# Kernel tuning notes

Measured on AMD Instinct MI355X. Metric: run time of the kernel, lower is better.

Reference implementation:

```python
import jax, jax.numpy as jnp
import numpy as np

DIM = 1024
HEADS = 16
HDIM = DIM // HEADS
MLP_HID = 4096
LN_EPS = 1e-5
NORM_EPS = 1e-12  # F.normalize eps


def _layernorm(x, g, b):
    mu = jnp.mean(x, axis=-1, keepdims=True)
    var = jnp.mean(jnp.square(x - mu), axis=-1, keepdims=True)
    return (x - mu) / jnp.sqrt(var + LN_EPS) * g + b


def _l2norm(x):
    n = jnp.linalg.norm(x, axis=-1, keepdims=True)
    return x / jnp.maximum(n, NORM_EPS)


def setup_inputs() -> dict:
    key = jax.random.key(0)
    ks = jax.random.split(key, 8)
    s = 0.02
    x = jax.random.normal(ks[0], (2, 2048, DIM), dtype=jnp.float32)
    w_qkv = jax.random.normal(ks[1], (3 * DIM, DIM), dtype=jnp.float32) * s  # torch Linear weight (out,in)
    w_proj = jax.random.normal(ks[2], (DIM, DIM), dtype=jnp.float32) * s
    temp = jnp.ones((HEADS, 1, 1), dtype=jnp.float32)
    w1 = jax.random.normal(ks[3], (MLP_HID, DIM), dtype=jnp.float32) * s
    b1 = jnp.zeros((MLP_HID,), dtype=jnp.float32)
    w2 = jax.random.normal(ks[4], (DIM, MLP_HID), dtype=jnp.float32) * s
    b2 = jnp.zeros((DIM,), dtype=jnp.float32)
    ln1_g = jnp.ones((DIM,), dtype=jnp.float32)
    ln1_b = jnp.zeros((DIM,), dtype=jnp.float32)
    ln2_g = jnp.ones((DIM,), dtype=jnp.float32)
    ln2_b = jnp.zeros((DIM,), dtype=jnp.float32)
    return {"x": x, "ln1_g": ln1_g, "ln1_b": ln1_b, "w_qkv": w_qkv,
            "w_proj": w_proj, "temp": temp, "ln2_g": ln2_g, "ln2_b": ln2_b,
            "w1": w1, "b1": b1, "w2": w2, "b2": b2}


def reference(x, ln1_g, ln1_b, w_qkv, w_proj, temp, ln2_g, ln2_b, w1, b1, w2, b2):
    b, n, c = x.shape
    # --- MHSA with L2-normalized q,k and learnable per-head temperature ---
    h = _layernorm(x, ln1_g, ln1_b)
    qkv = h @ w_qkv.T                             # [b,n,3c]
    qkv = qkv.reshape(b, n, 3, HEADS, HDIM).transpose(2, 0, 3, 1, 4)  # [3,b,h,n,d]
    q, k, v = qkv[0], qkv[1], qkv[2]
    q = _l2norm(q)
    k = _l2norm(k)
    attn = jnp.einsum('bhnd,bhmd->bhnm', q, k) * temp  # temp [h,1,1] broadcasts
    attn = jax.nn.softmax(attn, axis=-1)
    out = jnp.einsum('bhnm,bhmd->bhnd', attn, v)       # [b,h,n,d]
    out = out.transpose(0, 2, 1, 3).reshape(b, n, c)
    x = x + out @ w_proj.T
    # --- MLP ---
    h = _layernorm(x, ln2_g, ln2_b)
    h = jax.nn.gelu(h @ w1.T + b1, approximate=False)
    x = x + h @ w2.T + b2
    return x
```

## Files before the change

### kernel.cpp

```cpp
#include <hip/hip_runtime.h>
#include <cstdint>
#include <cstddef>

typedef unsigned short u16;
typedef __attribute__((ext_vector_type(8))) short short8;
typedef __attribute__((ext_vector_type(4))) float f32x4;
typedef __attribute__((ext_vector_type(4))) float float4v;
typedef __attribute__((ext_vector_type(4))) u16 u16x4;

__device__ __forceinline__ u16 f2bf(float f) {
  union { float f; uint32_t u; } v; v.f = f;
  uint32_t u = v.u;
  return (u16)((u + 0x7FFFu + ((u >> 16) & 1u)) >> 16);
}
__device__ __forceinline__ float bf2f(u16 s) {
  union { uint32_t u; float f; } v; v.u = ((uint32_t)s) << 16; return v.f;
}

__device__ __forceinline__ float fast_exp2(float x) {
#if __has_builtin(__builtin_amdgcn_exp2f)
  return __builtin_amdgcn_exp2f(x);
#else
  return exp2f(x);
#endif
}

__device__ __forceinline__ void gload16(const u16* g, u16* l) {
  __builtin_amdgcn_global_load_lds((const __attribute__((address_space(1))) void*)g,
                                   (__attribute__((address_space(3))) void*)l,
                                   16, 0, 0);
}

__global__ __launch_bounds__(256) void k_cvt(const float* __restrict__ in, u16* __restrict__ out, int n4) {
  int i = blockIdx.x * 256 + threadIdx.x;
  if (i >= n4) return;
  float4v v = *(const float4v*)(in + (size_t)i * 4);
  u16x4 o;
  #pragma unroll
  for (int j = 0; j < 4; j++) o[j] = f2bf(v[j]);
  *(u16x4*)(out + (size_t)i * 4) = o;
}

__global__ __launch_bounds__(256) void k_ln(const float* __restrict__ x, const float* __restrict__ g,
                                            const float* __restrict__ b, u16* __restrict__ out) {
  int row = blockIdx.x, tid = threadIdx.x;
  int wid = tid >> 6;
  const float* xr = x + (size_t)row * 1024;
  float4v v = *(const float4v*)(xr + tid * 4);
  float s = v[0] + v[1] + v[2] + v[3];
  float sq = v[0]*v[0] + v[1]*v[1] + v[2]*v[2] + v[3]*v[3];
  #pragma unroll
  for (int m = 1; m <= 32; m <<= 1) { s += __shfl_xor(s, m); sq += __shfl_xor(sq, m); }
  __shared__ float ss[4], ssq[4];
  if ((tid & 63) == 0) { ss[wid] = s; ssq[wid] = sq; }
  __syncthreads();
  s = ss[0] + ss[1] + ss[2] + ss[3];
  sq = ssq[0] + ssq[1] + ssq[2] + ssq[3];
  float mu = s * (1.0f/1024.0f);
  float var = sq * (1.0f/1024.0f) - mu*mu;
  float rs = rsqrtf(var + 1e-5f);
  u16x4 o;
  #pragma unroll
  for (int j = 0; j < 4; j++) {
    float y = (v[j] - mu) * rs * g[tid*4+j] + b[tid*4+j];
    o[j] = f2bf(y);
  }
  *(u16x4*)(out + (size_t)row * 1024 + tid * 4) = o;
}

__global__ __launch_bounds__(256) void k_redln(const float* __restrict__ x, const u16* __restrict__ P,
                                               const float* __restrict__ g, const float* __restrict__ b,
                                               float* __restrict__ x1, u16* __restrict__ h2) {
  int row = blockIdx.x, tid = threadIdx.x;
  int wid = tid >> 6;
  size_t off = (size_t)row * 1024 + tid * 4;
  float4v v = *(const float4v*)(x + off);
  #pragma unroll
  for (int z = 0; z < 4; z++) {
    u16x4 p = *(const u16x4*)(P + (size_t)z * 4194304 + off);
    #pragma unroll
    for (int j = 0; j < 4; j++) v[j] += bf2f(p[j]);
  }
  *(float4v*)(x1 + off) = v;
  float s = v[0] + v[1] + v[2] + v[3];
  float sq = v[0]*v[0] + v[1]*v[1] + v[2]*v[2] + v[3]*v[3];
  #pragma unroll
  for (int m = 1; m <= 32; m <<= 1) { s += __shfl_xor(s, m); sq += __shfl_xor(sq, m); }
  __shared__ float ss[4], ssq[4];
  if ((tid & 63) == 0) { ss[wid] = s; ssq[wid] = sq; }
  __syncthreads();
  s = ss[0] + ss[1] + ss[2] + ss[3];
  sq = ssq[0] + ssq[1] + ssq[2] + ssq[3];
  float mu = s * (1.0f/1024.0f);
  float var = sq * (1.0f/1024.0f) - mu*mu;
  float rs = rsqrtf(var + 1e-5f);
  u16x4 o;
  #pragma unroll
  for (int j = 0; j < 4; j++) o[j] = f2bf((v[j] - mu) * rs * g[tid*4+j] + b[tid*4+j]);
  *(u16x4*)(h2 + off) = o;
}

template<int EPI>
__global__ __launch_bounds__(512, 2) void k_g256(const u16* __restrict__ A, const u16* __restrict__ B,
                                                 const float* __restrict__ bias, u16* __restrict__ Cb,
                                                 int M, int N, int K, int Ksub) {
  extern __shared__ __align__(16) u16 smem[];
  int tid = threadIdx.x;
  int gx = gridDim.x;
  int lin = blockIdx.y * gx + blockIdx.x;
  int nwg = gx * gridDim.y;
  int cpx = nwg >> 3;
  int swz = (lin & 7) * cpx + (lin >> 3);
  int bx = swz % gx, by = swz / gx;
  int m0 = by * 256, n0 = bx * 256;
  int kbase = blockIdx.z * Ksub;
  int wid = tid >> 6, lane = tid & 63;
  int wm = wid >> 2, wn = wid & 3;
  int l15 = lane & 15, l16 = lane >> 4;

  f32x4 acc[8][4] = {};
  int nt = Ksub >> 5;

  auto STAGE = [&](int bsel, int kb) {
    u16* abase = smem + bsel * 16384;
    u16* bbase = abase + 8192;
    #pragma unroll
    for (int i = 0; i < 2; i++) {
      int c = i*512 + tid;
      int R = c >> 3, p = c & 7;
      int sp = p ^ (R & 7);
      int r = 2*R + (sp >> 2);
      int g = sp & 3;
      gload16(A + (size_t)(m0 + r)*K + kb + g*8, abase + c*8);
      gload16(B + (size_t)(n0 + r)*K + kb + g*8, bbase + c*8);
    }
  };

  STAGE(0, kbase);

  for (int t = 0; t < nt; ++t) {
    int sl = t & 1;
    asm volatile("s_waitcnt vmcnt(0)" ::: "memory");
    __builtin_amdgcn_sched_barrier(0);
    __builtin_amdgcn_s_barrier();
    __builtin_amdgcn_sched_barrier(0);
    if (t + 1 < nt) STAGE(sl ^ 1, kbase + (t + 1) * 32);
    const u16* ab = smem + sl * 16384;
    const u16* bb = ab + 8192;
    short8 af[8], bf[4];
    #pragma unroll
    for (int mf = 0; mf < 8; mf++) {
      int r = wm*128 + mf*16 + l15;
      int R = r >> 1;
      int sp = ((r & 1)*4 + l16) ^ (R & 7);
      af[mf] = *(const short8*)(ab + R*64 + sp*8);
    }
    #pragma unroll
    for (int nf = 0; nf < 4; nf++) {
      int r = wn*64 + nf*16 + l15;
      int R = r >> 1;
      int sp = ((r & 1)*4 + l16) ^ (R & 7);
      bf[nf] = *(const short8*)(bb + R*64 + sp*8);
    }
    asm volatile("s_waitcnt lgkmcnt(0)" ::: "memory");
    __builtin_amdgcn_sched_barrier(0);
    __builtin_amdgcn_s_setprio(1);
    #pragma unroll
    for (int mf = 0; mf < 8; mf++)
      #pragma unroll
      for (int nf = 0; nf < 4; nf++)
        acc[mf][nf] = __builtin_amdgcn_mfma_f32_16x16x32_bf16(af[mf], bf[nf], acc[mf][nf], 0, 0, 0);
    __builtin_amdgcn_s_setprio(0);
  }

  size_t zoff = (EPI == 6) ? (size_t)blockIdx.z * M * N : 0;
  #pragma unroll
  for (int mf = 0; mf < 8; mf++) {
    #pragma unroll
    for (int nf = 0; nf < 4; nf++) {
      int col = n0 + wn*64 + nf*16 + l15;
      #pragma unroll
      for (int r = 0; r < 4; r++) {
        int row = m0 + wm*128 + mf*16 + l16*4 + r;
        float v = acc[mf][nf][r];
        if constexpr (EPI == 2) { v += bias[col]; v = 0.5f*v*(1.0f + erff(v*0.70710678118f)); }
        Cb[zoff + (size_t)row*N + col] = f2bf(v);
      }
    }
  }
}

template<int HASB>
__global__ __launch_bounds__(256) void k_red4(const float* __restrict__ base, const float* __restrict__ bias,
                                              const u16* __restrict__ P, float* __restrict__ out) {
  int i = blockIdx.x * 256 + threadIdx.x;
  float4v v = *(const float4v*)(base + (size_t)i * 4);
  if constexpr (HASB) {
    float4v bb = *(const float4v*)(bias + (size_t)(i & 255) * 4);
    #pragma unroll
    for (int j = 0; j < 4; j++) v[j] += bb[j];
  }
  #pragma unroll
  for (int z = 0; z < 4; z++) {
    u16x4 p = *(const u16x4*)(P + (size_t)z * 4194304 + (size_t)i * 4);
    #pragma unroll
    for (int j = 0; j < 4; j++) v[j] += bf2f(p[j]);
  }
  *(float4v*)(out + (size_t)i * 4) = v;
}

__global__ __launch_bounds__(256) void k_prep(const u16* __restrict__ qkv, const float* __restrict__ temp,
                                              u16* __restrict__ Qn, u16* __restrict__ Kn, u16* __restrict__ Vt) {
  int grp = blockIdx.x, bh = blockIdx.y;
  int b = bh >> 4, h = bh & 15;
  int tid = threadIdx.x, wid = tid >> 6, lane = tid & 63;
  int n0 = grp * 64;
  __shared__ __align__(16) u16 vs[64*64];
  float tmp = temp[h] * 1.44269504f;
  for (int j = 0; j < 16; j++) {
    int tl = wid + 4*j;
    size_t roff = (size_t)((b*2048) + n0 + tl) * 3072;
    float q = bf2f(qkv[roff + h*64 + lane]);
    float k = bf2f(qkv[roff + 1024 + h*64 + lane]);
    u16 vraw = qkv[roff + 2048 + h*64 + lane];
    float sq = q*q, sk = k*k;
    #pragma unroll
    for (int m = 1; m <= 32; m <<= 1) { sq += __shfl_xor(sq, m); sk += __shfl_xor(sk, m); }
    float qs = tmp / fmaxf(sqrtf(sq), 1e-12f);
    float ksc = 1.0f / fmaxf(sqrtf(sk), 1e-12f);
    size_t obase = ((size_t)bh*2048 + n0 + tl)*64 + lane;
    Qn[obase] = f2bf(q * qs);
    Kn[obase] = f2bf(k * ksc);
    vs[tl*64 + lane] = vraw;
  }
  __syncthreads();
  int d = tid & 63, chunk = tid >> 6;
  u16 vals[16];
  #pragma unroll
  for (int jj = 0; jj < 16; jj++) vals[jj] = vs[(chunk*16 + jj)*64 + d];
  short8 w0, w1v;
  #pragma unroll
  for (int j = 0; j < 8; j++) { w0[j] = (short)vals[j]; w1v[j] = (short)vals[8+j]; }
  size_t vo = ((size_t)bh*64 + d)*2048 + n0 + chunk*16;
  *(short8*)(Vt + vo) = w0;
  *(short8*)(Vt + vo + 8) = w1v;
}

__device__ __forceinline__ int akey(int row) { return (row & 3) | (((row >> 3) & 1) << 2); }

__global__ __launch_bounds__(256) void k_attn(const u16* __restrict__ Qn, const u16* __restrict__ Kn,
                                              const u16* __restrict__ Vt, const float* __restrict__ temp,
                                              u16* __restrict__ Out) {
  __shared__ __align__(16) u16 Ks[2][64*64];
  __shared__ __align__(16) u16 Vs[2][64*64];
  int lin = blockIdx.y * gridDim.x + blockIdx.x;
  int c = lin & 7, t5 = lin >> 3;
  int bh = c*4 + (t5 >> 4);
  int qg = t5 & 15;
  int b = bh >> 4, h = bh & 15;
  int tid = threadIdx.x, wid = tid >> 6, lane = tid & 63;
  int l15 = lane & 15, l16 = lane >> 4;
  size_t base = (size_t)bh * 2048 * 64;
  size_t vbase = (size_t)bh * 64 * 2048;
  int q0 = qg*128 + wid*32;
  float m2 = fabsf(temp[h]) * 1.44269504f;
  short8 qf[2][2];
  #pragma unroll
  for (int g = 0; g < 2; g++)
    #pragma unroll
    for (int ks = 0; ks < 2; ks++)
      qf[g][ks] = *(const short8*)(Qn + base + (size_t)(q0 + g*16 + l15)*64 + ks*32 + l16*8);
  f32x4 o[2][4] = {};
  float lrow[2] = {0.f, 0.f};
  int prow = (l15 & 3) + 8*(l15 >> 2);

  auto STAGE = [&](int bsel, int kv0) {
    #pragma unroll
    for (int i = 0; i < 2; i++) {
      int cc = i*256 + tid;
      int row = cc >> 3, p = cc & 7;
      int g = p ^ akey(row);
      gload16(Kn + base + (size_t)(kv0 + row)*64 + g*8, &Ks[bsel][(i*256 + wid*64)*8]);
      gload16(Vt + vbase + (size_t)row*2048 + kv0 + g*8, &Vs[bsel][(i*256 + wid*64)*8]);
    }
  };

  STAGE(0, 0);
  __syncthreads();
  int cur = 0;
  for (int kv0 = 0; kv0 < 2048; kv0 += 64) {
    if (kv0 + 64 < 2048) STAGE(cur ^ 1, kv0 + 64);
    f32x4 s[2][4] = {};
    #pragma unroll
    for (int dks = 0; dks < 2; dks++) {
      #pragma unroll
      for (int ss = 0; ss < 4; ss++) {
        int row = (ss & 1)*4 + (ss >> 1)*32 + prow;
        short8 kf = *(const short8*)&Ks[cur][row*64 + ((dks*4 + l16) ^ akey(row))*8];
        s[0][ss] = __builtin_amdgcn_mfma_f32_16x16x32_bf16(kf, qf[0][dks], s[0][ss], 0, 0, 0);
        s[1][ss] = __builtin_amdgcn_mfma_f32_16x16x32_bf16(kf, qf[1][dks], s[1][ss], 0, 0, 0);
      }
    }
    short8 pf[2][2];
    #pragma unroll
    for (int g = 0; g < 2; g++) {
      float tsum = 0.f;
      #pragma unroll
      for (int kvs = 0; kvs < 2; kvs++) {
        float e[8];
        #pragma unroll
        for (int r = 0; r < 4; r++) {
          e[r]   = fast_exp2(s[g][kvs*2][r]   - m2);
          e[4+r] = fast_exp2(s[g][kvs*2+1][r] - m2);
        }
        #pragma unroll
        for (int r = 0; r < 8; r++) tsum += e[r];
        union { uint32_t u[4]; short8 v; } pu;
        #pragma unroll
        for (int w = 0; w < 4; w++) {
          uint32_t pk;
          asm("v_cvt_pk_bf16_f32 %0, %1, %2" : "=v"(pk) : "v"(e[2*w]), "v"(e[2*w+1]));
          pu.u[w] = pk;
        }
        pf[g][kvs] = pu.v;
      }
      lrow[g] += tsum;
    }
    #pragma unroll
    for (int kvs = 0; kvs < 2; kvs++) {
      short8 vf[4];
      #pragma unroll
      for (int dt = 0; dt < 4; dt++) {
        int row = dt*16 + l15;
        vf[dt] = *(const short8*)&Vs[cur][row*64 + (((kvs*4 + l16) ^ akey(row))*8)];
      }
      #pragma unroll
      for (int dt = 0; dt < 4; dt++) {
        o[0][dt] = __builtin_amdgcn_mfma_f32_16x16x32_bf16(vf[dt], pf[0][kvs], o[0][dt], 0, 0, 0);
        o[1][dt] = __builtin_amdgcn_mfma_f32_16x16x32_bf16(vf[dt], pf[1][kvs], o[1][dt], 0, 0, 0);
      }
    }
    __syncthreads();
    cur ^= 1;
  }
  #pragma unroll
  for (int g = 0; g < 2; g++) {
    float l = lrow[g];
    l += __shfl_xor(l, 16);
    l += __shfl_xor(l, 32);
    float rl = 1.0f / l;
    int tok = b*2048 + q0 + g*16 + l15;
    #pragma unroll
    for (int dt = 0; dt < 4; dt++) {
      u16x4 ov;
      #pragma unroll
      for (int r = 0; r < 4; r++) ov[r] = f2bf(o[g][dt][r] * rl);
      *(u16x4*)(Out + (size_t)tok*1024 + h*64 + dt*16 + l16*4) = ov;
    }
  }
}

static constexpr size_t OFF_WQKV  = 0;
static constexpr size_t OFF_WPROJ = OFF_WQKV  + 6291456;
static constexpr size_t OFF_W1    = OFF_WPROJ + 2097152;
static constexpr size_t OFF_W2    = OFF_W1    + 8388608;
static constexpr size_t OFF_HBF   = OFF_W2    + 8388608;
static constexpr size_t OFF_H2BF  = OFF_HBF   + 8388608;
static constexpr size_t OFF_QKVBF = OFF_H2BF  + 8388608;
static constexpr size_t OFF_QN    = OFF_QKVBF + 25165824;
static constexpr size_t OFF_KN    = OFF_QN    + 8388608;
static constexpr size_t OFF_VT    = OFF_KN    + 8388608;
static constexpr size_t OFF_AOUT  = OFF_VT    + 8388608;
static constexpr size_t OFF_X1    = OFF_AOUT  + 8388608;
static constexpr size_t OFF_HID   = OFF_X1    + 16777216;

extern "C" void kernel_launch(void* const* d_in, const int* in_sizes, int n_in,
                              void* d_out, int out_size, void* d_ws, size_t ws_size,
                              hipStream_t stream) {
  (void)in_sizes; (void)n_in; (void)out_size; (void)ws_size;
  const float* x     = (const float*)d_in[0];
  const float* ln1g  = (const float*)d_in[1];
  const float* ln1b  = (const float*)d_in[2];
  const float* wqkv  = (const float*)d_in[3];
  const float* wproj = (const float*)d_in[4];
  const float* temp  = (const float*)d_in[5];
  const float* ln2g  = (const float*)d_in[6];
  const float* ln2b  = (const float*)d_in[7];
  const float* w1    = (const float*)d_in[8];
  const float* b1    = (const float*)d_in[9];
  const float* w2    = (const float*)d_in[10];
  const float* b2    = (const float*)d_in[11];

  char* ws = (char*)d_ws;
  u16* wqkv_bf  = (u16*)(ws + OFF_WQKV);
  u16* wproj_bf = (u16*)(ws + OFF_WPROJ);
  u16* w1_bf    = (u16*)(ws + OFF_W1);
  u16* w2_bf    = (u16*)(ws + OFF_W2);
  u16* h_bf     = (u16*)(ws + OFF_HBF);
  u16* h2_bf    = (u16*)(ws + OFF_H2BF);
  u16* qkv_bf   = (u16*)(ws + OFF_QKVBF);
  u16* Qn       = (u16*)(ws + OFF_QN);
  u16* Kn       = (u16*)(ws + OFF_KN);
  u16* Vt       = (u16*)(ws + OFF_VT);
  u16* aout_bf  = (u16*)(ws + OFF_AOUT);
  float* x1     = (float*)(ws + OFF_X1);
  u16* hid_bf   = (u16*)(ws + OFF_HID);
  u16* part_p   = (u16*)(ws + OFF_HID);
  u16* part_m   = (u16*)(ws + OFF_QN);
  float* outf   = (float*)d_out;

  static bool attr_done = false;
  if (!attr_done) {
    hipFuncSetAttribute((const void*)k_g256<2>, hipFuncAttributeMaxDynamicSharedMemorySize, 65536);
    hipFuncSetAttribute((const void*)k_g256<4>, hipFuncAttributeMaxDynamicSharedMemorySize, 65536);
    hipFuncSetAttribute((const void*)k_g256<6>, hipFuncAttributeMaxDynamicSharedMemorySize, 65536);
    attr_done = true;
  }

  k_cvt<<<3072, 256, 0, stream>>>(wqkv,  wqkv_bf,  786432);
  k_cvt<<<1024, 256, 0, stream>>>(wproj, wproj_bf, 262144);
  k_cvt<<<4096, 256, 0, stream>>>(w1,    w1_bf,    1048576);
  k_cvt<<<4096, 256, 0, stream>>>(w2,    w2_bf,    1048576);

  k_ln<<<4096, 256, 0, stream>>>(x, ln1g, ln1b, h_bf);
  k_g256<4><<<dim3(12, 16), 512, 65536, stream>>>(h_bf, wqkv_bf, nullptr, qkv_bf, 4096, 3072, 1024, 1024);
  k_prep<<<dim3(32, 32), 256, 0, stream>>>(qkv_bf, temp, Qn, Kn, Vt);
  k_attn<<<dim3(16, 32), 256, 0, stream>>>(Qn, Kn, Vt, temp, aout_bf);
  k_g256<6><<<dim3(4, 16, 4), 512, 65536, stream>>>(aout_bf, wproj_bf, nullptr, part_p, 4096, 1024, 1024, 256);
  k_redln<<<4096, 256, 0, stream>>>(x, part_p, ln2g, ln2b, x1, h2_bf);
  k_g256<2><<<dim3(16, 16), 512, 65536, stream>>>(h2_bf, w1_bf, b1, hid_bf, 4096, 4096, 1024, 1024);
  k_g256<6><<<dim3(4, 16, 4), 512, 65536, stream>>>(hid_bf, w2_bf, nullptr, part_m, 4096, 1024, 4096, 1024);
  k_red4<1><<<4096, 256, 0, stream>>>(x1, b2, part_m, outf);
}
```

Measured before the change: 250.6 us.

## Rewrite GEMM main loop as 8-wave ping-pong with K=64 tiles and quartered MFMA phases

The 256x256 GEMM main loop now uses 64-wide K tiles in two LDS buffers of 64KB each, for 128KB of dynamic shared memory. Each tile is issued as four independent half-matrix load units interleaved with quarter-tile MFMA phases separated by barriers, in the style of HipKittens' 8-wave schedule. The aim is to overlap global loads, LDS reads and MFMA work more finely and to halve the barriers per K element. The cost is that 128KB of LDS per block likely drops occupancy to one block per CU despite launch_bounds(512,2), and many more barriers are issued per tile.

New measurement: 270.9 us. 1.08x slower.

```diff
diff --git a/kernel.cpp b/kernel.cpp
--- a/kernel.cpp
+++ b/kernel.cpp
@@ -99,6 +99,19 @@
   for (int j = 0; j < 4; j++) o[j] = f2bf((v[j] - mu) * rs * g[tid*4+j] + b[tid*4+j]);
   *(u16x4*)(h2 + off) = o;
 }
+
+#define SBAR __builtin_amdgcn_sched_barrier(0)
+#define BARR do { SBAR; __builtin_amdgcn_s_barrier(); SBAR; } while(0)
+#define LG0  do { asm volatile("s_waitcnt lgkmcnt(0)" ::: "memory"); SBAR; } while(0)
+#define VMW(n) do { asm volatile("s_waitcnt vmcnt(" #n ")" ::: "memory"); SBAR; } while(0)
+#define QMF(af_, bq_, mh_, nh_)                                                      \
+  do { __builtin_amdgcn_s_setprio(1);                                                \
+    _Pragma("unroll") for (int ks = 0; ks < 2; ks++)                                 \
+      _Pragma("unroll") for (int mf = 0; mf < 4; mf++)                               \
+        _Pragma("unroll") for (int nf = 0; nf < 2; nf++)                             \
+          acc[(mh_)*4+mf][(nh_)*2+nf] = __builtin_amdgcn_mfma_f32_16x16x32_bf16(     \
+            (af_)[mf*2+ks], (bq_)[nf*2+ks], acc[(mh_)*4+mf][(nh_)*2+nf], 0, 0, 0);   \
+    __builtin_amdgcn_s_setprio(0); } while(0)
 
 template<int EPI>
 __global__ __launch_bounds__(512, 2) void k_g256(const u16* __restrict__ A, const u16* __restrict__ B,
@@ -119,58 +132,78 @@
   int l15 = lane & 15, l16 = lane >> 4;
 
   f32x4 acc[8][4] = {};
-  int nt = Ksub >> 5;
-
-  auto STAGE = [&](int bsel, int kb) {
-    u16* abase = smem + bsel * 16384;
-    u16* bbase = abase + 8192;
-    #pragma unroll
-    for (int i = 0; i < 2; i++) {
-      int c = i*512 + tid;
+  int ntile = Ksub >> 6;
+  int nit = ntile >> 1;
+
+  auto UNIT = [&](int buf, int matsel, int half, int kt) {
+    const u16* src = matsel ? B : A;
+    int brow = (matsel ? n0 : m0) + half*128;
+    int kb = kbase + kt*64;
+    u16* dstb = smem + buf*32768 + matsel*16384 + half*8192;
+    #pragma unroll
+    for (int j = 0; j < 2; j++) {
+      int c = j*512 + wid*64 + lane;
       int R = c >> 3, p = c & 7;
-      int sp = p ^ (R & 7);
-      int r = 2*R + (sp >> 2);
-      int g = sp & 3;
-      gload16(A + (size_t)(m0 + r)*K + kb + g*8, abase + c*8);
-      gload16(B + (size_t)(n0 + r)*K + kb + g*8, bbase + c*8);
+      int g = p ^ (R & 7);
+      gload16(src + (size_t)(brow + R)*K + kb + g*8, dstb + (j*512 + wid*64)*8);
     }
   };
-
-  STAGE(0, kbase);
-
-  for (int t = 0; t < nt; ++t) {
-    int sl = t & 1;
-    asm volatile("s_waitcnt vmcnt(0)" ::: "memory");
-    __builtin_amdgcn_sched_barrier(0);
-    __builtin_amdgcn_s_barrier();
-    __builtin_amdgcn_sched_barrier(0);
-    if (t + 1 < nt) STAGE(sl ^ 1, kbase + (t + 1) * 32);
-    const u16* ab = smem + sl * 16384;
-    const u16* bb = ab + 8192;
-    short8 af[8], bf[4];
-    #pragma unroll
-    for (int mf = 0; mf < 8; mf++) {
-      int r = wm*128 + mf*16 + l15;
-      int R = r >> 1;
-      int sp = ((r & 1)*4 + l16) ^ (R & 7);
-      af[mf] = *(const short8*)(ab + R*64 + sp*8);
-    }
-    #pragma unroll
-    for (int nf = 0; nf < 4; nf++) {
-      int r = wn*64 + nf*16 + l15;
-      int R = r >> 1;
-      int sp = ((r & 1)*4 + l16) ^ (R & 7);
-      bf[nf] = *(const short8*)(bb + R*64 + sp*8);
-    }
-    asm volatile("s_waitcnt lgkmcnt(0)" ::: "memory");
-    __builtin_amdgcn_sched_barrier(0);
-    __builtin_amdgcn_s_setprio(1);
-    #pragma unroll
-    for (int mf = 0; mf < 8; mf++)
-      #pragma unroll
-      for (int nf = 0; nf < 4; nf++)
-        acc[mf][nf] = __builtin_amdgcn_mfma_f32_16x16x32_bf16(af[mf], bf[nf], acc[mf][nf], 0, 0, 0);
-    __builtin_amdgcn_s_setprio(0);
+  auto RDA = [&](short8* af, int buf, int mh) {
+    const u16* ab = smem + buf*32768;
+    #pragma unroll
+    for (int mf = 0; mf < 4; mf++)
+      #pragma unroll
+      for (int ks = 0; ks < 2; ks++) {
+        int r = wm*128 + (mh*4 + mf)*16 + l15;
+        int s = ks*4 + l16;
+        af[mf*2 + ks] = *(const short8*)(ab + r*64 + ((s ^ (r & 7))*8));
+      }
+  };
+  auto RDB = [&](short8* bq, int buf, int nh) {
+    const u16* bb = smem + buf*32768 + 16384;
+    #pragma unroll
+    for (int nf = 0; nf < 2; nf++)
+      #pragma unroll
+      for (int ks = 0; ks < 2; ks++) {
+        int r = wn*64 + (nh*2 + nf)*16 + l15;
+        int s = ks*4 + l16;
+        bq[nf*2 + ks] = *(const short8*)(bb + r*64 + ((s ^ (r & 7))*8));
+      }
+  };
+
+  UNIT(0,0,0,0); UNIT(0,0,1,0); UNIT(0,1,0,0); UNIT(0,1,1,0);
+  UNIT(1,0,0,1); UNIT(1,0,1,1); UNIT(1,1,0,1); UNIT(1,1,1,1);
+  VMW(8);
+  __builtin_amdgcn_s_barrier();
+  SBAR;
+
+  short8 afr[8], b0r[4], b1r[4];
+  for (int u = 0; u < nit; ++u) {
+    int tb = 2*u + 1, t2 = 2*u + 2, t3 = 2*u + 3;
+    bool sEarly = (u >= 1);
+    bool more = (t2 < ntile);
+    RDA(afr, 0, 0); RDB(b0r, 0, 0);
+    if (sEarly) UNIT(1, 0, 1, tb);
+    BARR; LG0; QMF(afr, b0r, 0, 0); BARR;
+    RDB(b1r, 0, 1);
+    if (sEarly) UNIT(1, 1, 0, tb);
+    BARR; LG0; QMF(afr, b1r, 0, 1); BARR;
+    RDA(afr, 0, 1);
+    if (sEarly) UNIT(1, 1, 1, tb);
+    BARR; LG0; QMF(afr, b1r, 1, 1); BARR;
+    if (more) { UNIT(0, 0, 0, t2); VMW(2); } else { VMW(0); }
+    BARR; QMF(afr, b0r, 1, 0); BARR;
+    RDA(afr, 1, 0); RDB(b0r, 1, 0);
+    if (more) UNIT(0, 0, 1, t2);
+    BARR; LG0; QMF(afr, b0r, 0, 0); BARR;
+    RDB(b1r, 1, 1);
+    if (more) UNIT(0, 1, 0, t2);
+    BARR; LG0; QMF(afr, b1r, 0, 1); BARR;
+    RDA(afr, 1, 1);
+    if (more) UNIT(0, 1, 1, t2);
+    BARR; LG0; QMF(afr, b1r, 1, 1); BARR;
+    if (more) { UNIT(1, 0, 0, t3); VMW(2); } else { VMW(0); }
+    BARR; QMF(afr, b0r, 1, 0); BARR;
   }
 
   size_t zoff = (EPI == 6) ? (size_t)blockIdx.z * M * N : 0;
@@ -411,9 +444,9 @@
 
   static bool attr_done = false;
   if (!attr_done) {
-    hipFuncSetAttribute((const void*)k_g256<2>, hipFuncAttributeMaxDynamicSharedMemorySize, 65536);
-    hipFuncSetAttribute((const void*)k_g256<4>, hipFuncAttributeMaxDynamicSharedMemorySize, 65536);
-    hipFuncSetAttribute((const void*)k_g256<6>, hipFuncAttributeMaxDynamicSharedMemorySize, 65536);
+    hipFuncSetAttribute((const void*)k_g256<2>, hipFuncAttributeMaxDynamicSharedMemorySize, 131072);
+    hipFuncSetAttribute((const void*)k_g256<4>, hipFuncAttributeMaxDynamicSharedMemorySize, 131072);
+    hipFuncSetAttribute((const void*)k_g256<6>, hipFuncAttributeMaxDynamicSharedMemorySize, 131072);
     attr_done = true;
   }
 
@@ -423,12 +456,12 @@
   k_cvt<<<4096, 256, 0, stream>>>(w2,    w2_bf,    1048576);
 
   k_ln<<<4096, 256, 0, stream>>>(x, ln1g, ln1b, h_bf);
-  k_g256<4><<<dim3(12, 16), 512, 65536, stream>>>(h_bf, wqkv_bf, nullptr, qkv_bf, 4096, 3072, 1024, 1024);
+  k_g256<4><<<dim3(12, 16), 512, 131072, stream>>>(h_bf, wqkv_bf, nullptr, qkv_bf, 4096, 3072, 1024, 1024);
   k_prep<<<dim3(32, 32), 256, 0, stream>>>(qkv_bf, temp, Qn, Kn, Vt);
   k_attn<<<dim3(16, 32), 256, 0, stream>>>(Qn, Kn, Vt, temp, aout_bf);
-  k_g256<6><<<dim3(4, 16, 4), 512, 65536, stream>>>(aout_bf, wproj_bf, nullptr, part_p, 4096, 1024, 1024, 256);
+  k_g256<6><<<dim3(4, 16, 4), 512, 131072, stream>>>(aout_bf, wproj_bf, nullptr, part_p, 4096, 1024, 1024, 256);
   k_redln<<<4096, 256, 0, stream>>>(x, part_p, ln2g, ln2b, x1, h2_bf);
-  k_g256<2><<<dim3(16, 16), 512, 65536, stream>>>(h2_bf, w1_bf, b1, hid_bf, 4096, 4096, 1024, 1024);
-  k_g256<6><<<dim3(4, 16, 4), 512, 65536, stream>>>(hid_bf, w2_bf, nullptr, part_m, 4096, 1024, 4096, 1024);
+  k_g256<2><<<dim3(16, 16), 512, 131072, stream>>>(h2_bf, w1_bf, b1, hid_bf, 4096, 4096, 1024, 1024);
+  k_g256<6><<<dim3(4, 16, 4), 512, 131072, stream>>>(hid_bf, w2_bf, nullptr, part_m, 4096, 1024, 4096, 1024);
   k_red4<1><<<4096, 256, 0, stream>>>(x1, b2, part_m, outf);
 }
```
